# Optimization experiments

Hardware: AMD Instinct MI355X
Metric: run time of the kernel (lower is better)

Reference implementation:

```python
import jax, jax.numpy as jnp
import numpy as np

BITS = 4
PACK = 32 // BITS  # 8 nibbles per int32
MASK = (1 << BITS) - 1


def _dequant_gptq(qweight, qzeros, scales):
    """GPTQ int4 dequantization matching MixedPrecisionLinear._dequantize_gptq_weight.

    qweight: [OC//PACK, IC] int32 (nibbles packed along output-channel rows)
    qzeros:  [G, IC//PACK]  int32 (nibbles packed along IC columns)
    scales:  [G, IC]        float32
    returns: [OC, IC]       float32 dequantized weight (pre-transpose)
    """
    Rp, IC = qweight.shape
    OC = Rp * PACK
    G = qzeros.shape[0]
    g = OC // G  # group size along OC

    # Unpack weights: row r*PACK + k comes from packed row r, shift k*BITS
    shifts = jnp.arange(PACK, dtype=jnp.int32) * BITS  # [PACK]
    Wq = ((qweight[:, None, :] >> shifts[None, :, None]) & MASK).reshape(OC, IC)

    # Unpack zero points per (group, ic)
    col = jnp.arange(IC, dtype=jnp.int32)
    qz_cols = qzeros[:, col // PACK]                       # [G, IC]
    zp = (qz_cols >> ((col % PACK) * BITS)[None, :]) & MASK  # [G, IC]

    zp_full = jnp.repeat(zp, g, axis=0)                    # [OC, IC]
    scales_full = jnp.repeat(scales, g, axis=0)            # [OC, IC]
    return (Wq - zp_full).astype(jnp.float32) * scales_full


def setup_inputs() -> dict:
    key = jax.random.key(0)
    k0, k1, k2, k3, k4 = jax.random.split(key, 5)
    IN, OUT, G = 4096, 11008, 32   # in_features (OC, packed), out_features (IC), groups
    N = 4096                        # flattened batch*seq tokens
    qweight = jax.random.randint(k0, (IN // PACK, OUT), 0, 2147483647, dtype=jnp.int32)
    qzeros = jax.random.randint(k1, (G, OUT // PACK), 0, 2147483647, dtype=jnp.int32)
    scales = jax.random.uniform(k2, (G, OUT), dtype=jnp.float32) * 0.01
    x = jax.random.normal(k3, (N, IN), dtype=jnp.float32)
    bias = jax.random.normal(k4, (OUT,), dtype=jnp.float32) * 0.01
    return {"input": x, "qweight": qweight, "qzeros": qzeros, "scales": scales, "bias": bias}


def reference(input, qweight, qzeros, scales, bias):
    # W_deq is [OC=in_features, IC=out_features]; the module returns W_deq.t() as the
    # linear weight, so F.linear(input, W_deq.t()) == input @ W_deq + bias.
    W = _dequant_gptq(qweight, qzeros, scales)
    return input @ W + bias
```

## Files before the change

### kernel.cpp

```cpp
#include <hip/hip_runtime.h>
#include <hip/hip_bf16.h>
#include <stdint.h>

#define M_DIM 4096
#define N_DIM 11008
#define K_DIM 4096

typedef float f32x4 __attribute__((ext_vector_type(4)));
typedef __bf16 bf16x8 __attribute__((ext_vector_type(8)));
typedef unsigned short u16x8 __attribute__((ext_vector_type(8)));
typedef unsigned short u16x4 __attribute__((ext_vector_type(4)));

typedef __attribute__((address_space(1))) const unsigned int guint;
typedef __attribute__((address_space(3))) unsigned int luint;
#define GLOAD_LDS16(g, l) \
    __builtin_amdgcn_global_load_lds((guint*)(g), (luint*)(l), 16, 0, 0)

#define WAIT_VM8() asm volatile("s_waitcnt vmcnt(8)" ::: "memory")
#define WAIT_VM4() asm volatile("s_waitcnt vmcnt(4)" ::: "memory")
#define WAIT_VM0() asm volatile("s_waitcnt vmcnt(0)" ::: "memory")

__device__ __forceinline__ unsigned short f2bf(float f) {
    union { float f; unsigned u; } v; v.f = f;
    return (unsigned short)((v.u + 0x7FFFu + ((v.u >> 16) & 1u)) >> 16);
}

__global__ void __launch_bounds__(256) cvt_x_kernel(
    const float* __restrict__ X, __hip_bfloat16* __restrict__ Y)
{
    const size_t i = ((size_t)blockIdx.x * 256 + threadIdx.x) * 8;
    f32x4 a = *reinterpret_cast<const f32x4*>(X + i);
    f32x4 b = *reinterpret_cast<const f32x4*>(X + i + 4);
    bf16x8 h;
    #pragma unroll
    for (int e = 0; e < 4; ++e) { h[e] = (__bf16)a[e]; h[e + 4] = (__bf16)b[e]; }
    *reinterpret_cast<bf16x8*>(Y + i) = h;
}

__global__ void __launch_bounds__(256) dequant_kernel(
    const int* __restrict__ QW, const int* __restrict__ QZ,
    const float* __restrict__ SC, __hip_bfloat16* __restrict__ Wt)
{
    const int n   = blockIdx.x * 64 + (threadIdx.x & 63);
    const int k64 = blockIdx.y * 4 + (threadIdx.x >> 6);
    const int g   = k64 >> 1;
    const int zp  = ((unsigned)QZ[g * (N_DIM / 8) + (n >> 3)] >> ((n & 7) << 2)) & 15;
    const float sc = SC[g * N_DIM + n];
    const float zs = (float)zp * sc;
    #pragma unroll
    for (int r = 0; r < 8; ++r) {
        const unsigned qw = (unsigned)QW[(size_t)(k64 * 8 + r) * N_DIM + n];
        bf16x8 h;
        #pragma unroll
        for (int j = 0; j < 8; ++j)
            h[j] = (__bf16)((float)((qw >> (j * 4)) & 15u) * sc - zs);
        *reinterpret_cast<bf16x8*>(Wt + (size_t)n * K_DIM + k64 * 64 + r * 8) = h;
    }
}

__global__ void __launch_bounds__(512, 2) gemm_bf16_kernel(
    const __hip_bfloat16* __restrict__ A,
    const __hip_bfloat16* __restrict__ Bt,
    const float* __restrict__ BIAS, float* __restrict__ OUT)
{
    extern __shared__ unsigned char lds[];

    const int tid  = threadIdx.x;
    const int wave = tid >> 6;
    const int lane = tid & 63;
    const int l15  = lane & 15;
    const int lhi  = lane >> 4;
    const int wr   = wave >> 2;
    const int wc   = wave & 3;

    const int bid = blockIdx.x;
    const int swz = (bid & 7) * 86 + (bid >> 3);
    const int m0  = (swz & 15) * 256;
    const int n0  = (swz >> 4) * 256;

    const int pp  = tid >> 3;
    const int so  = (tid & 7) ^ (pp & 7);
    const int grow = pp * 2 + (so >> 2);
    const int klo  = (so & 3) * 8;
    const __hip_bfloat16* Asrc = A  + (size_t)(m0 + grow) * K_DIM + klo;
    const __hip_bfloat16* Bsrc = Bt + (size_t)(n0 + grow) * K_DIM + klo;
    const int t16 = tid * 16;

    const int sws   = (((l15 & 1) << 2) | lhi) ^ ((l15 >> 1) & 7);
    const int lbase = (l15 >> 1) * 128 + sws * 16;
    int aoff[8], boff[4];
    #pragma unroll
    for (int fr = 0; fr < 8; ++fr)
        aoff[fr] = (wr * 128 + fr * 16) * 64 + lbase;
    #pragma unroll
    for (int fc = 0; fc < 4; ++fc)
        boff[fc] = (wc * 64 + fc * 16) * 64 + lbase;

    f32x4 acc[8][4] = {};

    auto stA0 = [&](int c) {
        const int sb = (c & 1) * 65536; const size_t k = (size_t)c * 64;
        GLOAD_LDS16(Asrc + k,                        lds + sb + t16);
        GLOAD_LDS16(Asrc + k + (size_t)128 * K_DIM,  lds + sb + 8192 + t16);
    };
    auto stB0 = [&](int c) {
        const int sb = (c & 1) * 65536; const size_t k = (size_t)c * 64;
        GLOAD_LDS16(Bsrc + k,                        lds + sb + 32768 + t16);
        GLOAD_LDS16(Bsrc + k + (size_t)128 * K_DIM,  lds + sb + 32768 + 8192 + t16);
    };
    auto stA1 = [&](int c) {
        const int sb = (c & 1) * 65536; const size_t k = (size_t)c * 64 + 32;
        GLOAD_LDS16(Asrc + k,                        lds + sb + 16384 + t16);
        GLOAD_LDS16(Asrc + k + (size_t)128 * K_DIM,  lds + sb + 16384 + 8192 + t16);
    };
    auto stB1 = [&](int c) {
        const int sb = (c & 1) * 65536; const size_t k = (size_t)c * 64 + 32;
        GLOAD_LDS16(Bsrc + k,                        lds + sb + 49152 + t16);
        GLOAD_LDS16(Bsrc + k + (size_t)128 * K_DIM,  lds + sb + 49152 + 8192 + t16);
    };

    auto tile = [&](int c, bool st, bool tail) {
        const int buf = (c & 1) * 65536;
        bf16x8 afr[4], bfr[4];
        #pragma unroll
        for (int fc = 0; fc < 4; ++fc)
            bfr[fc] = *reinterpret_cast<const bf16x8*>(lds + buf + 32768 + boff[fc]);
        #pragma unroll
        for (int fr = 0; fr < 4; ++fr)
            afr[fr] = *reinterpret_cast<const bf16x8*>(lds + buf + aoff[fr]);
        if (st) stA0(c + 1);
        __builtin_amdgcn_s_barrier();
        __builtin_amdgcn_s_setprio(1);
        #pragma unroll
        for (int fr = 0; fr < 4; ++fr)
            #pragma unroll
            for (int fc = 0; fc < 4; ++fc)
                acc[fr][fc] = __builtin_amdgcn_mfma_f32_16x16x32_bf16(
                    afr[fr], bfr[fc], acc[fr][fc], 0, 0, 0);
        __builtin_amdgcn_s_setprio(0);
        #pragma unroll
        for (int fr = 0; fr < 4; ++fr)
            afr[fr] = *reinterpret_cast<const bf16x8*>(lds + buf + aoff[fr + 4]);
        if (st) stB0(c + 1);
        if (tail) { WAIT_VM0(); } else { WAIT_VM4(); }
        __builtin_amdgcn_s_barrier();
        __builtin_amdgcn_s_setprio(1);
        #pragma unroll
        for (int fr = 0; fr < 4; ++fr)
            #pragma unroll
            for (int fc = 0; fc < 4; ++fc)
                acc[fr + 4][fc] = __builtin_amdgcn_mfma_f32_16x16x32_bf16(
                    afr[fr], bfr[fc], acc[fr + 4][fc], 0, 0, 0);
        __builtin_amdgcn_s_setprio(0);
        #pragma unroll
        for (int fc = 0; fc < 4; ++fc)
            bfr[fc] = *reinterpret_cast<const bf16x8*>(lds + buf + 49152 + boff[fc]);
        #pragma unroll
        for (int fr = 0; fr < 4; ++fr)
            afr[fr] = *reinterpret_cast<const bf16x8*>(lds + buf + 16384 + aoff[fr]);
        if (st) stA1(c + 1);
        __builtin_amdgcn_s_barrier();
        __builtin_amdgcn_s_setprio(1);
        #pragma unroll
        for (int fr = 0; fr < 4; ++fr)
            #pragma unroll
            for (int fc = 0; fc < 4; ++fc)
                acc[fr][fc] = __builtin_amdgcn_mfma_f32_16x16x32_bf16(
                    afr[fr], bfr[fc], acc[fr][fc], 0, 0, 0);
        __builtin_amdgcn_s_setprio(0);
        #pragma unroll
        for (int fr = 0; fr < 4; ++fr)
            afr[fr] = *reinterpret_cast<const bf16x8*>(lds + buf + 16384 + aoff[fr + 4]);
        if (st) stB1(c + 1);
        if (!tail) { WAIT_VM4(); }
        __builtin_amdgcn_s_barrier();
        __builtin_amdgcn_s_setprio(1);
        #pragma unroll
        for (int fr = 0; fr < 4; ++fr)
            #pragma unroll
            for (int fc = 0; fc < 4; ++fc)
                acc[fr + 4][fc] = __builtin_amdgcn_mfma_f32_16x16x32_bf16(
                    afr[fr], bfr[fc], acc[fr + 4][fc], 0, 0, 0);
        __builtin_amdgcn_s_setprio(0);
    };

    stA0(0); stB0(0); stA1(0); stB1(0);
    WAIT_VM4();
    __builtin_amdgcn_s_barrier();

    for (int c = 0; c <= 62; ++c)
        tile(c, true, false);
    tile(63, false, true);

    #pragma unroll
    for (int fc = 0; fc < 4; ++fc) {
        const int n    = n0 + wc * 64 + fc * 16 + l15;
        const float bv = BIAS[n];
        #pragma unroll
        for (int fr = 0; fr < 8; ++fr) {
            const int mb = m0 + wr * 128 + fr * 16 + (lhi << 2);
            #pragma unroll
            for (int t = 0; t < 4; ++t)
                OUT[(size_t)(mb + t) * N_DIM + n] = acc[fr][fc][t] + bv;
        }
    }
}

__global__ void __launch_bounds__(256) gptq_gemm_kernel(
    const float* __restrict__ X, const int* __restrict__ QW,
    const int* __restrict__ QZ, const float* __restrict__ SC,
    const float* __restrict__ BIAS, float* __restrict__ OUT)
{
    __shared__ __align__(16) unsigned char slds[32768];
    const int tid  = threadIdx.x;
    const int n0   = blockIdx.x * 128;
    const int m0   = blockIdx.y * 128;
    const int wave = tid >> 6;
    const int lane = tid & 63;
    const int wm   = (wave >> 1) * 64;
    const int wn   = (wave & 1) * 64;
    const int l15  = lane & 15;
    const int lhi  = lane >> 4;
    const int arow  = tid >> 4;
    const int acol4 = (tid & 15) << 2;
    const int bnl   = tid & 127;
    const int brb   = tid >> 7;
    const int col   = n0 + bnl;

    f32x4 acc[4][4] = {};
    for (int kt = 0; kt < K_DIM / 64; ++kt) {
        const int k0 = kt * 64;
        #pragma unroll
        for (int r8 = 0; r8 < 8; ++r8) {
            const int row = (r8 << 4) + arow;
            f32x4 v = *reinterpret_cast<const f32x4*>(
                X + (size_t)(m0 + row) * K_DIM + (k0 + acol4));
            u16x4 h;
            #pragma unroll
            for (int e = 0; e < 4; ++e) h[e] = f2bf(v[e]);
            const int bo = row * 128 + ((acol4 << 1) ^ ((row & 7) << 4));
            *reinterpret_cast<u16x4*>(slds + bo) = h;
        }
        {
            const int g    = k0 >> 7;
            const int zp   = (((unsigned)QZ[g * (N_DIM / 8) + (col >> 3)])
                              >> ((col & 7) << 2)) & 15;
            const float sc = SC[g * N_DIM + col];
            const float zs = (float)zp * sc;
            #pragma unroll
            for (int rb = 0; rb < 4; ++rb) {
                const int rl = (rb << 1) + brb;
                const unsigned qw =
                    (unsigned)QW[(size_t)((k0 >> 3) + rl) * N_DIM + col];
                u16x8 h;
                #pragma unroll
                for (int j = 0; j < 8; ++j) {
                    float w = (float)((qw >> (j << 2)) & 15u) * sc - zs;
                    h[j] = f2bf(w);
                }
                const int bo = 16384 + bnl * 128 + ((rl << 4) ^ ((bnl & 7) << 4));
                *reinterpret_cast<u16x8*>(slds + bo) = h;
            }
        }
        __syncthreads();
        #pragma unroll
        for (int kk = 0; kk < 2; ++kk) {
            bf16x8 afr[4], bfr[4];
            #pragma unroll
            for (int i = 0; i < 4; ++i) {
                const int row = wm + (i << 4) + l15;
                afr[i] = *reinterpret_cast<const bf16x8*>(
                    slds + row * 128 + (((kk << 6) + (lhi << 4)) ^ ((row & 7) << 4)));
            }
            #pragma unroll
            for (int j = 0; j < 4; ++j) {
                const int n = wn + (j << 4) + l15;
                bfr[j] = *reinterpret_cast<const bf16x8*>(
                    slds + 16384 + n * 128 + (((kk << 6) + (lhi << 4)) ^ ((n & 7) << 4)));
            }
            #pragma unroll
            for (int i = 0; i < 4; ++i)
                #pragma unroll
                for (int j = 0; j < 4; ++j)
                    acc[i][j] = __builtin_amdgcn_mfma_f32_16x16x32_bf16(
                        afr[i], bfr[j], acc[i][j], 0, 0, 0);
        }
        __syncthreads();
    }
    #pragma unroll
    for (int j = 0; j < 4; ++j) {
        const int n    = n0 + wn + (j << 4) + l15;
        const float bv = BIAS[n];
        #pragma unroll
        for (int i = 0; i < 4; ++i) {
            const int mb = m0 + wm + (i << 4) + (lhi << 2);
            #pragma unroll
            for (int t = 0; t < 4; ++t)
                OUT[(size_t)(mb + t) * N_DIM + n] = acc[i][j][t] + bv;
        }
    }
}

extern "C" void kernel_launch(void* const* d_in, const int* in_sizes, int n_in,
                              void* d_out, int out_size, void* d_ws, size_t ws_size,
                              hipStream_t stream) {
    const float* X  = (const float*)d_in[0];
    const int*   QW = (const int*)d_in[1];
    const int*   QZ = (const int*)d_in[2];
    const float* SC = (const float*)d_in[3];
    const float* BI = (const float*)d_in[4];
    float*      OUT = (float*)d_out;

    const size_t xbf_bytes = (size_t)M_DIM * K_DIM * 2;
    const size_t wt_bytes  = (size_t)N_DIM * K_DIM * 2;

    if (ws_size >= xbf_bytes + wt_bytes) {
        __hip_bfloat16* Xbf = (__hip_bfloat16*)d_ws;
        __hip_bfloat16* Wt  = (__hip_bfloat16*)((char*)d_ws + xbf_bytes);

        cvt_x_kernel<<<(M_DIM * K_DIM) / (256 * 8), 256, 0, stream>>>(X, Xbf);
        dequant_kernel<<<dim3(N_DIM / 64, K_DIM / 256), 256, 0, stream>>>(QW, QZ, SC, Wt);
        gemm_bf16_kernel<<<dim3((M_DIM / 256) * (N_DIM / 256)), 512, 131072, stream>>>(
            Xbf, Wt, BI, OUT);
    } else {
        gptq_gemm_kernel<<<dim3(N_DIM / 128, M_DIM / 128), 256, 0, stream>>>(
            X, QW, QZ, SC, BI, OUT);
    }
}
```

Baseline: 408.3 us.

## Switch GEMM inner loop to 32x32x16 bf16 MFMA with new LDS fragment layout

Replaces the 16x16x32 MFMA tiling (8x4 fragments per wave) with 32x32x16 MFMA instructions (4x2 fragments per wave, two k-substeps per 32-wide slice), recomputing the swizzled LDS read offsets and the output store mapping. Larger MFMA tiles mean fewer LDS fragment reads per FLOP and fewer MFMA issues. The trade-off is longer-latency instructions and a trickier store layout, and a mistake in the offset or row mapping would give wrong results.

```diff
diff --git a/kernel.cpp b/kernel.cpp
--- a/kernel.cpp
+++ b/kernel.cpp
@@ -7,6 +7,7 @@
 #define K_DIM 4096
 
 typedef float f32x4 __attribute__((ext_vector_type(4)));
+typedef float f32x16 __attribute__((ext_vector_type(16)));
 typedef __bf16 bf16x8 __attribute__((ext_vector_type(8)));
 typedef unsigned short u16x8 __attribute__((ext_vector_type(8)));
 typedef unsigned short u16x4 __attribute__((ext_vector_type(4)));
@@ -16,7 +17,6 @@
 #define GLOAD_LDS16(g, l) \
     __builtin_amdgcn_global_load_lds((guint*)(g), (luint*)(l), 16, 0, 0)
 
-#define WAIT_VM8() asm volatile("s_waitcnt vmcnt(8)" ::: "memory")
 #define WAIT_VM4() asm volatile("s_waitcnt vmcnt(4)" ::: "memory")
 #define WAIT_VM0() asm volatile("s_waitcnt vmcnt(0)" ::: "memory")
 
@@ -68,8 +68,8 @@
     const int tid  = threadIdx.x;
     const int wave = tid >> 6;
     const int lane = tid & 63;
-    const int l15  = lane & 15;
-    const int lhi  = lane >> 4;
+    const int l31  = lane & 31;
+    const int khb  = lane >> 5;
     const int wr   = wave >> 2;
     const int wc   = wave & 3;
 
@@ -86,17 +86,25 @@
     const __hip_bfloat16* Bsrc = Bt + (size_t)(n0 + grow) * K_DIM + klo;
     const int t16 = tid * 16;
 
-    const int sws   = (((l15 & 1) << 2) | lhi) ^ ((l15 >> 1) & 7);
-    const int lbase = (l15 >> 1) * 128 + sws * 16;
-    int aoff[8], boff[4];
-    #pragma unroll
-    for (int fr = 0; fr < 8; ++fr)
-        aoff[fr] = (wr * 128 + fr * 16) * 64 + lbase;
-    #pragma unroll
-    for (int fc = 0; fc < 4; ++fc)
-        boff[fc] = (wc * 64 + fc * 16) * 64 + lbase;
-
-    f32x4 acc[8][4] = {};
+    const int r2  = l31 >> 1;
+    const int par = (l31 & 1) << 2;
+    const int q0  = ((par | khb)       ^ (r2 & 7)) << 4;
+    const int q1  = ((par | (2 | khb)) ^ (r2 & 7)) << 4;
+    int aoff[4][2], boff[2][2];
+    #pragma unroll
+    for (int fr = 0; fr < 4; ++fr) {
+        const int pr = wr * 64 + fr * 16 + r2;
+        aoff[fr][0] = pr * 128 + q0;
+        aoff[fr][1] = pr * 128 + q1;
+    }
+    #pragma unroll
+    for (int fc = 0; fc < 2; ++fc) {
+        const int pr = wc * 32 + fc * 16 + r2;
+        boff[fc][0] = 32768 + pr * 128 + q0;
+        boff[fc][1] = 32768 + pr * 128 + q1;
+    }
+
+    f32x16 acc[4][2] = {};
 
     auto stA0 = [&](int c) {
         const int sb = (c & 1) * 65536; const size_t k = (size_t)c * 64;
@@ -121,66 +129,86 @@
 
     auto tile = [&](int c, bool st, bool tail) {
         const int buf = (c & 1) * 65536;
-        bf16x8 afr[4], bfr[4];
-        #pragma unroll
-        for (int fc = 0; fc < 4; ++fc)
-            bfr[fc] = *reinterpret_cast<const bf16x8*>(lds + buf + 32768 + boff[fc]);
-        #pragma unroll
-        for (int fr = 0; fr < 4; ++fr)
-            afr[fr] = *reinterpret_cast<const bf16x8*>(lds + buf + aoff[fr]);
+        bf16x8 afr[2][2], bfr[2][2];
+        #pragma unroll
+        for (int fc = 0; fc < 2; ++fc) {
+            bfr[fc][0] = *reinterpret_cast<const bf16x8*>(lds + buf + boff[fc][0]);
+            bfr[fc][1] = *reinterpret_cast<const bf16x8*>(lds + buf + boff[fc][1]);
+        }
+        #pragma unroll
+        for (int fr = 0; fr < 2; ++fr) {
+            afr[fr][0] = *reinterpret_cast<const bf16x8*>(lds + buf + aoff[fr][0]);
+            afr[fr][1] = *reinterpret_cast<const bf16x8*>(lds + buf + aoff[fr][1]);
+        }
         if (st) stA0(c + 1);
         __builtin_amdgcn_s_barrier();
         __builtin_amdgcn_s_setprio(1);
         #pragma unroll
-        for (int fr = 0; fr < 4; ++fr)
-            #pragma unroll
-            for (int fc = 0; fc < 4; ++fc)
-                acc[fr][fc] = __builtin_amdgcn_mfma_f32_16x16x32_bf16(
-                    afr[fr], bfr[fc], acc[fr][fc], 0, 0, 0);
+        for (int ks = 0; ks < 2; ++ks)
+            #pragma unroll
+            for (int fr = 0; fr < 2; ++fr)
+                #pragma unroll
+                for (int fc = 0; fc < 2; ++fc)
+                    acc[fr][fc] = __builtin_amdgcn_mfma_f32_32x32x16_bf16(
+                        afr[fr][ks], bfr[fc][ks], acc[fr][fc], 0, 0, 0);
         __builtin_amdgcn_s_setprio(0);
         #pragma unroll
-        for (int fr = 0; fr < 4; ++fr)
-            afr[fr] = *reinterpret_cast<const bf16x8*>(lds + buf + aoff[fr + 4]);
+        for (int fr = 0; fr < 2; ++fr) {
+            afr[fr][0] = *reinterpret_cast<const bf16x8*>(lds + buf + aoff[fr + 2][0]);
+            afr[fr][1] = *reinterpret_cast<const bf16x8*>(lds + buf + aoff[fr + 2][1]);
+        }
         if (st) stB0(c + 1);
         if (tail) { WAIT_VM0(); } else { WAIT_VM4(); }
         __builtin_amdgcn_s_barrier();
         __builtin_amdgcn_s_setprio(1);
         #pragma unroll
-        for (int fr = 0; fr < 4; ++fr)
-            #pragma unroll
-            for (int fc = 0; fc < 4; ++fc)
-                acc[fr + 4][fc] = __builtin_amdgcn_mfma_f32_16x16x32_bf16(
-                    afr[fr], bfr[fc], acc[fr + 4][fc], 0, 0, 0);
+        for (int ks = 0; ks < 2; ++ks)
+            #pragma unroll
+            for (int fr = 0; fr < 2; ++fr)
+                #pragma unroll
+                for (int fc = 0; fc < 2; ++fc)
+                    acc[fr + 2][fc] = __builtin_amdgcn_mfma_f32_32x32x16_bf16(
+                        afr[fr][ks], bfr[fc][ks], acc[fr + 2][fc], 0, 0, 0);
         __builtin_amdgcn_s_setprio(0);
         #pragma unroll
-        for (int fc = 0; fc < 4; ++fc)
-            bfr[fc] = *reinterpret_cast<const bf16x8*>(lds + buf + 49152 + boff[fc]);
-        #pragma unroll
-        for (int fr = 0; fr < 4; ++fr)
-            afr[fr] = *reinterpret_cast<const bf16x8*>(lds + buf + 16384 + aoff[fr]);
+        for (int fc = 0; fc < 2; ++fc) {
+            bfr[fc][0] = *reinterpret_cast<const bf16x8*>(lds + buf + 16384 + boff[fc][0]);
+            bfr[fc][1] = *reinterpret_cast<const bf16x8*>(lds + buf + 16384 + boff[fc][1]);
+        }
+        #pragma unroll
+        for (int fr = 0; fr < 2; ++fr) {
+            afr[fr][0] = *reinterpret_cast<const bf16x8*>(lds + buf + 16384 + aoff[fr][0]);
+            afr[fr][1] = *reinterpret_cast<const bf16x8*>(lds + buf + 16384 + aoff[fr][1]);
+        }
         if (st) stA1(c + 1);
         __builtin_amdgcn_s_barrier();
         __builtin_amdgcn_s_setprio(1);
         #pragma unroll
-        for (int fr = 0; fr < 4; ++fr)
-            #pragma unroll
-            for (int fc = 0; fc < 4; ++fc)
-                acc[fr][fc] = __builtin_amdgcn_mfma_f32_16x16x32_bf16(
-                    afr[fr], bfr[fc], acc[fr][fc], 0, 0, 0);
+        for (int ks = 0; ks < 2; ++ks)
+            #pragma unroll
+            for (int fr = 0; fr < 2; ++fr)
+                #pragma unroll
+                for (int fc = 0; fc < 2; ++fc)
+                    acc[fr][fc] = __builtin_amdgcn_mfma_f32_32x32x16_bf16(
+                        afr[fr][ks], bfr[fc][ks], acc[fr][fc], 0, 0, 0);
         __builtin_amdgcn_s_setprio(0);
         #pragma unroll
-        for (int fr = 0; fr < 4; ++fr)
-            afr[fr] = *reinterpret_cast<const bf16x8*>(lds + buf + 16384 + aoff[fr + 4]);
+        for (int fr = 0; fr < 2; ++fr) {
+            afr[fr][0] = *reinterpret_cast<const bf16x8*>(lds + buf + 16384 + aoff[fr + 2][0]);
+            afr[fr][1] = *reinterpret_cast<const bf16x8*>(lds + buf + 16384 + aoff[fr + 2][1]);
+        }
         if (st) stB1(c + 1);
         if (!tail) { WAIT_VM4(); }
         __builtin_amdgcn_s_barrier();
         __builtin_amdgcn_s_setprio(1);
         #pragma unroll
-        for (int fr = 0; fr < 4; ++fr)
-            #pragma unroll
-            for (int fc = 0; fc < 4; ++fc)
-                acc[fr + 4][fc] = __builtin_amdgcn_mfma_f32_16x16x32_bf16(
-                    afr[fr], bfr[fc], acc[fr + 4][fc], 0, 0, 0);
+        for (int ks = 0; ks < 2; ++ks)
+            #pragma unroll
+            for (int fr = 0; fr < 2; ++fr)
+                #pragma unroll
+                for (int fc = 0; fc < 2; ++fc)
+                    acc[fr + 2][fc] = __builtin_amdgcn_mfma_f32_32x32x16_bf16(
+                        afr[fr][ks], bfr[fc][ks], acc[fr + 2][fc], 0, 0, 0);
         __builtin_amdgcn_s_setprio(0);
     };
 
@@ -193,15 +221,17 @@
     tile(63, false, true);
 
     #pragma unroll
-    for (int fc = 0; fc < 4; ++fc) {
-        const int n    = n0 + wc * 64 + fc * 16 + l15;
+    for (int fc = 0; fc < 2; ++fc) {
+        const int n    = n0 + wc * 64 + fc * 32 + l31;
         const float bv = BIAS[n];
         #pragma unroll
-        for (int fr = 0; fr < 8; ++fr) {
-            const int mb = m0 + wr * 128 + fr * 16 + (lhi << 2);
-            #pragma unroll
-            for (int t = 0; t < 4; ++t)
-                OUT[(size_t)(mb + t) * N_DIM + n] = acc[fr][fc][t] + bv;
+        for (int fr = 0; fr < 4; ++fr) {
+            const int mb = m0 + wr * 128 + fr * 32 + 4 * khb;
+            #pragma unroll
+            for (int reg = 0; reg < 16; ++reg) {
+                const int m = mb + (reg & 3) + 8 * (reg >> 2);
+                OUT[(size_t)m * N_DIM + n] = acc[fr][fc][reg] + bv;
+            }
         }
     }
 }
```

After: 415.6 us. No clear change (+1.8%).
